# Optimization experiments

Hardware: AMD Instinct MI355X
Metric: run time of the kernel (lower is better)

The kernel has to match this reference:

```python
import jax, jax.numpy as jnp
import numpy as np

B, L, H, D = 2, 2048, 16, 64
HID = H * D
EPS = 1e-6


def setup_inputs() -> dict:
    key = jax.random.key(0)
    k1, k2, k3 = jax.random.split(key, 3)
    x = jax.random.normal(k1, (B, L, HID), dtype=jnp.float32)
    Wqkv = jax.random.normal(k2, (HID, 3 * HID), dtype=jnp.float32) * 0.02
    Wo = jax.random.normal(k3, (HID, HID), dtype=jnp.float32) * 0.02
    q_norm_w = jnp.ones((D,), dtype=jnp.float32)
    k_norm_w = jnp.ones((D,), dtype=jnp.float32)
    # real RoPE tables: (L, D/2)
    d2 = D // 2
    inv_freq = 1.0 / (10000.0 ** (np.arange(d2, dtype=np.float32) / d2))
    ang = np.arange(L, dtype=np.float32)[:, None] * inv_freq[None, :]
    cos = jnp.asarray(np.cos(ang), dtype=jnp.float32)
    sin = jnp.asarray(np.sin(ang), dtype=jnp.float32)
    return {"x": x, "Wqkv": Wqkv, "Wo": Wo, "q_norm_w": q_norm_w,
            "k_norm_w": k_norm_w, "cos": cos, "sin": sin}


def _rmsnorm(t, w, eps=EPS):
    # normalize over last (head_dim) axis
    var = jnp.mean(t * t, axis=-1, keepdims=True)
    return t * jax.lax.rsqrt(var + eps) * w


def _rope(t, cos, sin):
    # t: (B,H,L,D); cos,sin: (1,1,L,D/2)
    d2 = t.shape[-1] // 2
    t1, t2 = t[..., :d2], t[..., d2:]
    return jnp.concatenate([t1 * cos - t2 * sin, t1 * sin + t2 * cos], axis=-1)


def reference(x, Wqkv, Wo, q_norm_w, k_norm_w, cos, sin):
    Bx, Lx, _ = x.shape
    qkv = x @ Wqkv                                   # (B,L,3*HID)
    qkv = qkv.reshape(Bx, Lx, 3, H, D)
    q = jnp.transpose(qkv[:, :, 0], (0, 2, 1, 3))    # (B,H,L,D)
    k = jnp.transpose(qkv[:, :, 1], (0, 2, 1, 3))
    v = jnp.transpose(qkv[:, :, 2], (0, 2, 1, 3))
    q = _rmsnorm(q, q_norm_w)
    k = _rmsnorm(k, k_norm_w)
    c = cos[:Lx][None, None]                         # (1,1,L,D/2)
    s = sin[:Lx][None, None]
    q = _rope(q, c, s)
    k = _rope(k, c, s)
    scale = 1.0 / jnp.sqrt(jnp.float32(D))
    scores = jnp.einsum("bhqd,bhkd->bhqk", q, k) * scale
    causal = jnp.tril(jnp.ones((Lx, Lx), dtype=bool))
    scores = jnp.where(causal, scores, jnp.finfo(scores.dtype).min)
    attn = jax.nn.softmax(scores, axis=-1)
    out = jnp.einsum("bhqk,bhkd->bhqd", attn, v)     # (B,H,L,D)
    out = jnp.transpose(out, (0, 2, 1, 3)).reshape(Bx, Lx, HID)
    return out @ Wo
```

## Files before the change

### kernel.cpp

```cpp
#include <hip/hip_runtime.h>
#include <hip/hip_bf16.h>

typedef __attribute__((ext_vector_type(8))) short bh8;
typedef __attribute__((ext_vector_type(4))) float f4;

typedef unsigned short u16;
typedef unsigned int u32;

__device__ inline u16 f2b(float f) {
  __hip_bfloat16 h = __float2bfloat16(f);
  union { __hip_bfloat16 h; u16 u; } v; v.h = h; return v.u;
}
__device__ inline float b2f(u16 b) {
  union { u32 u; float f; } v; v.u = ((u32)b) << 16;
  return v.f;
}

__device__ __forceinline__ void gload16(const u16* g, u16* l) {
  __builtin_amdgcn_global_load_lds(
      (__attribute__((address_space(1))) void*)(g),
      (__attribute__((address_space(3))) void*)(l),
      16, 0, 0);
}

__global__ __launch_bounds__(256) void k_prep1(const float* __restrict__ x,
                                               const float* __restrict__ Wqkv,
                                               const float* __restrict__ Wo,
                                               u16* __restrict__ xb,
                                               u16* __restrict__ wqkvT,
                                               u16* __restrict__ woT) {
  int idx = blockIdx.x;
  if (idx < 4096) {
    int i = (idx * 256 + threadIdx.x) * 4;
    float4 v = *(const float4*)&x[i];
    ushort4 o;
    o.x = f2b(v.x); o.y = f2b(v.y); o.z = f2b(v.z); o.w = f2b(v.w);
    *(ushort4*)&xb[i] = o;
    return;
  }
  __shared__ u16 t[32][33];
  const float* W; u16* WT; int K, N, bxi, byi;
  if (idx < 7168) {
    int id2 = idx - 4096;
    W = Wqkv; WT = wqkvT; K = 1024; N = 3072;
    bxi = id2 % 96; byi = id2 / 96;
  } else {
    int id2 = idx - 7168;
    W = Wo; WT = woT; K = 1024; N = 1024;
    bxi = id2 & 31; byi = id2 >> 5;
  }
  int bx = bxi * 32, by = byi * 32;
  int xx = threadIdx.x & 31, yy = threadIdx.x >> 5;
  for (int j = 0; j < 4; ++j) {
    int r = yy + j * 8;
    t[r][xx] = f2b(W[(size_t)(by + r) * N + bx + xx]);
  }
  __syncthreads();
  for (int j = 0; j < 4; ++j) {
    int r = yy + j * 8;
    WT[(size_t)(bx + r) * K + by + xx] = t[xx][r];
  }
}

template <bool F32OUT>
__global__ __launch_bounds__(512, 2) void k_gemm256(const u16* __restrict__ A,
                                                    const u16* __restrict__ Bt,
                                                    void* __restrict__ Cout,
                                                    int M, int N, int K) {
  __shared__ u16 As[2][2][128 * 64];
  __shared__ u16 Bs[2][2][128 * 64];
  const int tid = threadIdx.x;
  const int lane = tid & 63, wid = tid >> 6;
  const int l15 = lane & 15, lg = lane >> 4;
  const int wm = wid >> 2, wn = wid & 3;

  int nwg = gridDim.x * gridDim.y;
  int bid = blockIdx.y * gridDim.x + blockIdx.x;
  int cpx = nwg >> 3;
  int swz = (bid & 7) * cpx + (bid >> 3);
  int bx = swz % gridDim.x, by = swz / gridDim.x;
  const int bm = bx * 256, bn = by * 256;

  f4 acc[8][4] = {};

  const int srow = wid * 16 + (lane >> 3);
  const int key0 = (lane >> 3) & 7;
  const int scol = ((lane & 7) ^ key0) * 8;

  const int nk = K >> 6;

#define STAGE256(T)                                                                   \
  {                                                                                   \
    int kb_ = (T) << 6; int bf_ = (T) & 1;                                            \
    _Pragma("unroll")                                                                 \
    for (int h = 0; h < 2; ++h) {                                                     \
      const u16* ga = A + (size_t)(bm + h * 128 + srow) * K + kb_ + scol;             \
      u16* la = &As[bf_][h][(wid * 16) * 64];                                         \
      gload16(ga, la);                                                                \
      gload16(ga + (size_t)8 * K, la + 8 * 64);                                       \
      const u16* gb = Bt + (size_t)(bn + h * 128 + srow) * K + kb_ + scol;            \
      u16* lb = &Bs[bf_][h][(wid * 16) * 64];                                         \
      gload16(gb, lb);                                                                \
      gload16(gb + (size_t)8 * K, lb + 8 * 64);                                       \
    }                                                                                 \
  }

#define QUAD256(T, MH, NH)                                                            \
  {                                                                                   \
    const u16* as_ = &As[(T) & 1][wm][0];                                             \
    const u16* bs_ = &Bs[(T) & 1][wn >> 1][0];                                        \
    bh8 a_[4][2], b_[2][2];                                                           \
    _Pragma("unroll")                                                                 \
    for (int i = 0; i < 4; ++i) {                                                     \
      int ar = ((MH) * 4 + i) * 16 + l15;                                             \
      _Pragma("unroll")                                                               \
      for (int kk = 0; kk < 2; ++kk)                                                  \
        a_[i][kk] = *(const bh8*)&as_[ar * 64 + (((kk * 4 + lg) ^ (ar & 7)) * 8)];    \
    }                                                                                 \
    _Pragma("unroll")                                                                 \
    for (int j = 0; j < 2; ++j) {                                                     \
      int br = (wn & 1) * 64 + ((NH) * 2 + j) * 16 + l15;                             \
      _Pragma("unroll")                                                               \
      for (int kk = 0; kk < 2; ++kk)                                                  \
        b_[j][kk] = *(const bh8*)&bs_[br * 64 + (((kk * 4 + lg) ^ (br & 7)) * 8)];    \
    }                                                                                 \
    asm volatile("s_waitcnt lgkmcnt(0)" ::: "memory");                                \
    __builtin_amdgcn_sched_barrier(0);                                                \
    __builtin_amdgcn_s_setprio(1);                                                    \
    _Pragma("unroll")                                                                 \
    for (int kk = 0; kk < 2; ++kk)                                                    \
      _Pragma("unroll")                                                               \
      for (int i = 0; i < 4; ++i)                                                     \
        _Pragma("unroll")                                                             \
        for (int j = 0; j < 2; ++j)                                                   \
          acc[(MH) * 4 + i][(NH) * 2 + j] = __builtin_amdgcn_mfma_f32_16x16x32_bf16(  \
              a_[i][kk], b_[j][kk], acc[(MH) * 4 + i][(NH) * 2 + j], 0, 0, 0);        \
    __builtin_amdgcn_s_setprio(0);                                                    \
  }

  STAGE256(0);
  __syncthreads();

  for (int t = 0; t < nk; ++t) {
    if (t + 1 < nk) STAGE256(t + 1);
    QUAD256(t, 0, 0);
    QUAD256(t, 0, 1);
    QUAD256(t, 1, 0);
    QUAD256(t, 1, 1);
    __syncthreads();
  }
#undef STAGE256
#undef QUAD256

  for (int mf = 0; mf < 8; ++mf)
    for (int nf = 0; nf < 4; ++nf)
      for (int r = 0; r < 4; ++r) {
        int row = bm + wm * 128 + mf * 16 + lg * 4 + r;
        int col = bn + wn * 64 + nf * 16 + l15;
        float v = acc[mf][nf][r];
        if constexpr (F32OUT) ((float*)Cout)[(size_t)row * N + col] = v;
        else                  ((u16*)Cout)[(size_t)row * N + col]  = f2b(v);
      }
}

template <bool F32OUT>
__global__ __launch_bounds__(256) void k_gemm(const u16* __restrict__ A,
                                              const u16* __restrict__ Bt,
                                              void* __restrict__ Cout,
                                              int M, int N, int K) {
  __shared__ u16 As[2][128 * 64];
  __shared__ u16 Bs[2][128 * 64];
  const int tid = threadIdx.x;
  const int lane = tid & 63, wid = tid >> 6;
  const int l15 = lane & 15, lg = lane >> 4;
  const int bm = blockIdx.x * 128, bn = blockIdx.y * 128;
  const int wr = (wid >> 1) * 64, wc = (wid & 1) * 64;

  f4 acc[4][4] = {};

  const int srow = wid * 32 + (lane >> 3);
  const int scol = (lane & 7) * 8;
  const u16* gA = A  + (size_t)(bm + srow) * K + scol;
  const u16* gB = Bt + (size_t)(bn + srow) * K + scol;

  const int nk = K >> 6;

  {
    const u16* ga = gA; const u16* gb = gB;
    u16* la = &As[0][(wid * 32) * 64];
    u16* lb = &Bs[0][(wid * 32) * 64];
    #pragma unroll
    for (int c = 0; c < 4; ++c) {
      gload16(ga, la);
      gload16(gb, lb);
      ga += (size_t)8 * K; gb += (size_t)8 * K;
      la += 8 * 64;        lb += 8 * 64;
    }
  }
  __syncthreads();

  for (int t = 0; t < nk; ++t) {
    if (t + 1 < nk) {
      int kb = (t + 1) << 6;
      const u16* ga = gA + kb; const u16* gb = gB + kb;
      u16* la = &As[(t + 1) & 1][(wid * 32) * 64];
      u16* lb = &Bs[(t + 1) & 1][(wid * 32) * 64];
      #pragma unroll
      for (int c = 0; c < 4; ++c) {
        gload16(ga, la);
        gload16(gb, lb);
        ga += (size_t)8 * K; gb += (size_t)8 * K;
        la += 8 * 64;        lb += 8 * 64;
      }
    }
    const u16* as = &As[t & 1][0];
    const u16* bs = &Bs[t & 1][0];
    #pragma unroll
    for (int kk = 0; kk < 2; ++kk) {
      bh8 a[4], b[4];
      #pragma unroll
      for (int m = 0; m < 4; ++m)
        a[m] = *(const bh8*)&as[(wr + m * 16 + l15) * 64 + kk * 32 + lg * 8];
      #pragma unroll
      for (int n = 0; n < 4; ++n)
        b[n] = *(const bh8*)&bs[(wc + n * 16 + l15) * 64 + kk * 32 + lg * 8];
      #pragma unroll
      for (int m = 0; m < 4; ++m)
        #pragma unroll
        for (int n = 0; n < 4; ++n)
          acc[m][n] = __builtin_amdgcn_mfma_f32_16x16x32_bf16(a[m], b[n], acc[m][n], 0, 0, 0);
    }
    __syncthreads();
  }

  for (int m = 0; m < 4; ++m)
    for (int n = 0; n < 4; ++n)
      for (int r = 0; r < 4; ++r) {
        int row = bm + wr + m * 16 + lg * 4 + r;
        int col = bn + wc + n * 16 + l15;
        float v = acc[m][n][r];
        if constexpr (F32OUT) ((float*)Cout)[(size_t)row * N + col] = v;
        else                  ((u16*)Cout)[(size_t)row * N + col]  = f2b(v);
      }
}

__global__ __launch_bounds__(256) void k_prep2(const u16* __restrict__ qkv,
                                               const float* __restrict__ qw,
                                               const float* __restrict__ kw,
                                               const float* __restrict__ cosp,
                                               const float* __restrict__ sinp,
                                               u16* __restrict__ Q,
                                               u16* __restrict__ K,
                                               u16* __restrict__ Vt) {
  const float CSC = 0.125f * 1.44269504088896f;
  int idx = blockIdx.x;
  if (idx < 2048) {
    int wid = threadIdx.x >> 6, lane = threadIdx.x & 63;
    int gw = idx * 4 + wid;
    int isK = gw & 1;
    int bl = gw >> 1;
    int l = bl & 2047, b = bl >> 11;
    int h = lane >> 2, qd = lane & 3;
    const u16* src = qkv + (size_t)bl * 3072 + isK * 1024 + h * 64 + qd * 8;
    bh8 t1 = *(const bh8*)src;
    bh8 t2 = *(const bh8*)(src + 32);
    float a1[8], a2[8];
    float ss = 0.0f;
    #pragma unroll
    for (int j = 0; j < 8; ++j) {
      a1[j] = b2f((u16)t1[j]); a2[j] = b2f((u16)t2[j]);
      ss += a1[j] * a1[j] + a2[j] * a2[j];
    }
    ss += __shfl_xor(ss, 1, 64);
    ss += __shfl_xor(ss, 2, 64);
    float rr = rsqrtf(ss * (1.0f / 64.0f) + 1e-6f);
    const float* wt = isK ? kw : qw;
    float w1[8], w2[8], cc[8], sn[8];
    *(float4*)&w1[0] = *(const float4*)&wt[qd * 8];
    *(float4*)&w1[4] = *(const float4*)&wt[qd * 8 + 4];
    *(float4*)&w2[0] = *(const float4*)&wt[32 + qd * 8];
    *(float4*)&w2[4] = *(const float4*)&wt[32 + qd * 8 + 4];
    *(float4*)&cc[0] = *(const float4*)&cosp[l * 32 + qd * 8];
    *(float4*)&cc[4] = *(const float4*)&cosp[l * 32 + qd * 8 + 4];
    *(float4*)&sn[0] = *(const float4*)&sinp[l * 32 + qd * 8];
    *(float4*)&sn[4] = *(const float4*)&sinp[l * 32 + qd * 8 + 4];
    float scl = isK ? 1.0f : CSC;
    bh8 o1, o2;
    #pragma unroll
    for (int j = 0; j < 8; ++j) {
      float x1 = a1[j] * rr * w1[j];
      float x2 = a2[j] * rr * w2[j];
      o1[j] = (short)f2b((x1 * cc[j] - x2 * sn[j]) * scl);
      o2[j] = (short)f2b((x1 * sn[j] + x2 * cc[j]) * scl);
    }
    u16* dst = (isK ? K : Q) + ((size_t)(b * 16 + h) * 2048 + l) * 64 + qd * 8;
    *(bh8*)dst = o1;
    *(bh8*)(dst + 32) = o2;
  } else {
    __shared__ u16 t[32][33];
    int v = idx - 2048;
    int bxi = v & 63, byi = (v >> 6) & 1, bh = v >> 7;
    int b = bh >> 4, h = bh & 15;
    int lb = bxi * 32, db = byi * 32;
    int xx = threadIdx.x & 31, yy = threadIdx.x >> 5;
    const u16* src = qkv + (size_t)b * 2048 * 3072 + 2048 + h * 64;
    for (int j = 0; j < 4; ++j) {
      int r = yy + j * 8;
      t[r][xx] = src[(size_t)(lb + r) * 3072 + db + xx];
    }
    __syncthreads();
    u16* dst = Vt + (size_t)bh * 64 * 2048;
    for (int j = 0; j < 4; ++j) {
      int r = yy + j * 8;
      dst[(size_t)(db + r) * 2048 + lb + xx] = t[xx][r];
    }
  }
}

__global__ __launch_bounds__(256, 3) void k_attn(const u16* __restrict__ Q,
                                                 const u16* __restrict__ K,
                                                 const u16* __restrict__ Vt,
                                                 u16* __restrict__ O,
                                                 u16* __restrict__ Opart,
                                                 float2* __restrict__ Ml) {
  __shared__ u16 Ks[2][64 * 64];
  __shared__ u16 Vs[2][64 * 64];
  __shared__ u16 Pl[4][32][64];

  const int bh = blockIdx.y;
  const int b = bh >> 4, h = bh & 15;
  const int wid = threadIdx.x >> 6, lane = threadIdx.x & 63;
  const int l15 = lane & 15, lg = lane >> 4;

  const int id = 39 - (int)blockIdx.x;
  int qt, t0, t1, slot;
  if (id < 4) { qt = id; t0 = 0; t1 = 2 * qt + 2; slot = -1; }
  else if (id < 12) {
    int p = id - 4; qt = 4 + (p >> 1); int half = p & 1;
    int nt = qt + 1; t0 = half * nt; t1 = t0 + nt;
    slot = bh * 36 + (qt - 4) * 2 + half;
  } else if (id < 24) {
    int p = id - 12; qt = 8 + p / 3; int part = p % 3;
    int T = 2 * qt + 2; t0 = part * T / 3; t1 = (part + 1) * T / 3;
    slot = bh * 36 + 8 + (qt - 8) * 3 + part;
  } else {
    int p = id - 24; qt = 12 + (p >> 2); int part = p & 3;
    int T = 2 * qt + 2; t0 = part * T / 4; t1 = (part + 1) * T / 4;
    slot = bh * 36 + 20 + (qt - 12) * 4 + part;
  }
  const int qb = qt * 128 + wid * 32;

  const u16* Qp = Q  + (size_t)bh * 2048 * 64;
  const u16* Kp = K  + (size_t)bh * 2048 * 64;
  const u16* Vp = Vt + (size_t)bh * 64 * 2048;

  const int sr0 = wid * 8 + (lane >> 3);
  const int sc  = lane & 7;

  bh8 aq[2][2];
  #pragma unroll
  for (int qi = 0; qi < 2; ++qi)
    #pragma unroll
    for (int hh = 0; hh < 2; ++hh)
      aq[qi][hh] = *(const bh8*)&Qp[(size_t)(qb + qi * 16 + l15) * 64 + hh * 32 + lg * 8];

  bh8 ones;
  #pragma unroll
  for (int j = 0; j < 8; ++j) ones[j] = (short)0x3F80;

  f4 acc[2][4] = {};
  float mrow[2] = {-1e30f, -1e30f};
  float lrow[2] = {0.0f, 0.0f};

  const int tmax = (qb + 31) >> 6;

  {
    int kb0 = t0 * 64;
    int r0 = sr0, r1 = 32 + sr0;
    gload16(Kp + (size_t)(kb0 + r0) * 64 + (size_t)((sc ^ (r0 & 7)) * 8), &Ks[t0 & 1][(wid * 8) * 64]);
    gload16(Kp + (size_t)(kb0 + r1) * 64 + (size_t)((sc ^ (r1 & 7)) * 8), &Ks[t0 & 1][(32 + wid * 8) * 64]);
    gload16(Vp + (size_t)r0 * 2048 + kb0 + (size_t)((sc ^ (r0 & 7)) * 8), &Vs[t0 & 1][(wid * 8) * 64]);
    gload16(Vp + (size_t)r1 * 2048 + kb0 + (size_t)((sc ^ (r1 & 7)) * 8), &Vs[t0 & 1][(32 + wid * 8) * 64]);
  }
  __syncthreads();

  for (int t = t0; t < t1; ++t) {
    if (t + 1 < t1) {
      int kb = (t + 1) * 64;
      int nb = (t + 1) & 1;
      int r0 = sr0, r1 = 32 + sr0;
      gload16(Kp + (size_t)(kb + r0) * 64 + (size_t)((sc ^ (r0 & 7)) * 8), &Ks[nb][(wid * 8) * 64]);
      gload16(Kp + (size_t)(kb + r1) * 64 + (size_t)((sc ^ (r1 & 7)) * 8), &Ks[nb][(32 + wid * 8) * 64]);
      gload16(Vp + (size_t)r0 * 2048 + kb + (size_t)((sc ^ (r0 & 7)) * 8), &Vs[nb][(wid * 8) * 64]);
      gload16(Vp + (size_t)r1 * 2048 + kb + (size_t)((sc ^ (r1 & 7)) * 8), &Vs[nb][(32 + wid * 8) * 64]);
    }
    if (t <= tmax) {
      const int kb = t * 64;
      const bool masked = (t == tmax);
      const u16* ks = &Ks[t & 1][0];
      const u16* vs = &Vs[t & 1][0];

      f4 sc4[4][2] = {};
      __builtin_amdgcn_s_setprio(1);
      #pragma unroll
      for (int kq = 0; kq < 4; ++kq) {
        int row = kq * 16 + l15;
        int cs = row & 7;
        bh8 ka0 = *(const bh8*)&ks[row * 64 + ((0 + lg) ^ cs) * 8];
        bh8 ka1 = *(const bh8*)&ks[row * 64 + ((4 + lg) ^ cs) * 8];
        #pragma unroll
        for (int qi = 0; qi < 2; ++qi) {
          sc4[kq][qi] = __builtin_amdgcn_mfma_f32_16x16x32_bf16(ka0, aq[qi][0], sc4[kq][qi], 0, 0, 0);
          sc4[kq][qi] = __builtin_amdgcn_mfma_f32_16x16x32_bf16(ka1, aq[qi][1], sc4[kq][qi], 0, 0, 0);
        }
      }
      __builtin_amdgcn_s_setprio(0);

      #pragma unroll
      for (int qi = 0; qi < 2; ++qi) {
        if (masked) {
          int q = qb + qi * 16 + l15;
          #pragma unroll
          for (int kq = 0; kq < 4; ++kq)
            #pragma unroll
            for (int r = 0; r < 4; ++r)
              if (kb + kq * 16 + lg * 4 + r > q) sc4[kq][qi][r] = -1e30f;
        }
        float mx = -1e30f;
        #pragma unroll
        for (int kq = 0; kq < 4; ++kq)
          #pragma unroll
          for (int r = 0; r < 4; ++r)
            mx = fmaxf(mx, sc4[kq][qi][r]);
        mx = fmaxf(mx, __shfl_xor(mx, 16, 64));
        mx = fmaxf(mx, __shfl_xor(mx, 32, 64));
        if (__any(mx > mrow[qi] + 8.0f)) {
          float mnew = fmaxf(mrow[qi], mx);
          float fac = exp2f(mrow[qi] - mnew);
          mrow[qi] = mnew;
          lrow[qi] *= fac;
          #pragma unroll
          for (int n = 0; n < 4; ++n)
            #pragma unroll
            for (int r = 0; r < 4; ++r) acc[qi][n][r] *= fac;
        }
        #pragma unroll
        for (int kq = 0; kq < 4; ++kq)
          #pragma unroll
          for (int r = 0; r < 4; ++r)
            sc4[kq][qi][r] = exp2f(sc4[kq][qi][r] - mrow[qi]);
      }

      char* plb = (char*)&Pl[wid][0][0];
      #pragma unroll
      for (int qi = 0; qi < 2; ++qi) {
        int row = qi * 16 + l15;
        #pragma unroll
        for (int kq = 0; kq < 4; ++kq) {
          ushort4 w4;
          w4.x = f2b(sc4[kq][qi][0]); w4.y = f2b(sc4[kq][qi][1]);
          w4.z = f2b(sc4[kq][qi][2]); w4.w = f2b(sc4[kq][qi][3]);
          int ch = (kq * 2 + (lg >> 1)) ^ (row & 7);
          *(ushort4*)(plb + row * 128 + ch * 16 + (lg & 1) * 8) = w4;
        }
      }
      asm volatile("s_waitcnt lgkmcnt(0)" ::: "memory");
      __builtin_amdgcn_sched_barrier(0);

      f4 sum0 = {}, sum1 = {};
      __builtin_amdgcn_s_setprio(1);
      #pragma unroll
      for (int g = 0; g < 2; ++g) {
        bh8 pb0 = *(const bh8*)(plb + l15 * 128 + (((g * 4 + lg) ^ (l15 & 7)) * 16));
        bh8 pb1 = *(const bh8*)(plb + (16 + l15) * 128 + (((g * 4 + lg) ^ (l15 & 7)) * 16));
        #pragma unroll
        for (int n = 0; n < 4; ++n) {
          int row = n * 16 + l15;
          bh8 va = *(const bh8*)&vs[row * 64 + (((g * 4 + lg) ^ (row & 7)) * 8)];
          acc[0][n] = __builtin_amdgcn_mfma_f32_16x16x32_bf16(va, pb0, acc[0][n], 0, 0, 0);
          acc[1][n] = __builtin_amdgcn_mfma_f32_16x16x32_bf16(va, pb1, acc[1][n], 0, 0, 0);
        }
        sum0 = __builtin_amdgcn_mfma_f32_16x16x32_bf16(ones, pb0, sum0, 0, 0, 0);
        sum1 = __builtin_amdgcn_mfma_f32_16x16x32_bf16(ones, pb1, sum1, 0, 0, 0);
      }
      __builtin_amdgcn_s_setprio(0);
      lrow[0] += sum0[0];
      lrow[1] += sum1[0];
    }
    __syncthreads();
  }

  if (slot < 0) {
    #pragma unroll
    for (int qi = 0; qi < 2; ++qi) {
      float inv = 1.0f / lrow[qi];
      int q = qb + qi * 16 + l15;
      #pragma unroll
      for (int n = 0; n < 4; ++n) {
        ushort4 w4;
        w4.x = f2b(acc[qi][n][0] * inv);
        w4.y = f2b(acc[qi][n][1] * inv);
        w4.z = f2b(acc[qi][n][2] * inv);
        w4.w = f2b(acc[qi][n][3] * inv);
        *(ushort4*)&O[((size_t)b * 2048 + q) * 1024 + h * 64 + n * 16 + lg * 4] = w4;
      }
    }
  } else {
    u16* op = Opart + (size_t)slot * 8192;
    #pragma unroll
    for (int qi = 0; qi < 2; ++qi) {
      int rloc = wid * 32 + qi * 16 + l15;
      #pragma unroll
      for (int n = 0; n < 4; ++n) {
        ushort4 w4;
        w4.x = f2b(acc[qi][n][0]); w4.y = f2b(acc[qi][n][1]);
        w4.z = f2b(acc[qi][n][2]); w4.w = f2b(acc[qi][n][3]);
        *(ushort4*)&op[(size_t)rloc * 64 + n * 16 + lg * 4] = w4;
      }
      if (lg == 0) Ml[slot * 128 + rloc] = make_float2(mrow[qi], lrow[qi]);
    }
  }
}

__global__ __launch_bounds__(256) void k_comb(const u16* __restrict__ Opart,
                                              const float2* __restrict__ Ml,
                                              u16* __restrict__ O) {
  int qt = 4 + (int)blockIdx.x;
  int bh = blockIdx.y;
  int b = bh >> 4, h = bh & 15;
  int ways = qt < 8 ? 2 : (qt < 12 ? 3 : 4);
  int base = bh * 36 + (qt < 8 ? (qt - 4) * 2 : qt < 12 ? 8 + (qt - 8) * 3 : 20 + (qt - 12) * 4);
  int row = threadIdx.x >> 1;
  int db  = (threadIdx.x & 1) * 32;

  float2 ml[4]; float wgt[4];
  float M = -1e30f;
  #pragma unroll
  for (int w = 0; w < 4; ++w)
    if (w < ways) { ml[w] = Ml[(base + w) * 128 + row]; M = fmaxf(M, ml[w].x); }
  float l = 0.0f;
  #pragma unroll
  for (int w = 0; w < 4; ++w)
    if (w < ways) { wgt[w] = exp2f(ml[w].x - M); l += wgt[w] * ml[w].y; }
  float inv = 1.0f / l;

  u16* dst = O + ((size_t)b * 2048 + qt * 128 + row) * 1024 + h * 64 + db;
  #pragma unroll
  for (int j = 0; j < 32; j += 8) {
    float a[8] = {};
    #pragma unroll
    for (int w = 0; w < 4; ++w)
      if (w < ways) {
        bh8 v = *(const bh8*)&Opart[(size_t)(base + w) * 8192 + (size_t)row * 64 + db + j];
        #pragma unroll
        for (int e = 0; e < 8; ++e) a[e] += wgt[w] * b2f((u16)v[e]);
      }
    bh8 o;
    #pragma unroll
    for (int e = 0; e < 8; ++e) o[e] = (short)f2b(a[e] * inv);
    *(bh8*)&dst[j] = o;
  }
}

extern "C" void kernel_launch(void* const* d_in, const int* in_sizes, int n_in,
                              void* d_out, int out_size, void* d_ws, size_t ws_size,
                              hipStream_t stream) {
  (void)in_sizes; (void)n_in; (void)out_size; (void)ws_size;
  const float* x    = (const float*)d_in[0];
  const float* Wqkv = (const float*)d_in[1];
  const float* Wo   = (const float*)d_in[2];
  const float* qw   = (const float*)d_in[3];
  const float* kw   = (const float*)d_in[4];
  const float* cosp = (const float*)d_in[5];
  const float* sinp = (const float*)d_in[6];
  float* out = (float*)d_out;

  char* ws = (char*)d_ws;
  u16* xb    = (u16*)(ws);
  u16* wqkvT = (u16*)(ws + 8388608);
  u16* woT   = (u16*)(ws + 14680064);
  u16* qkv   = (u16*)(ws + 16777216);
  u16* Qb    = (u16*)(ws + 41943040);
  u16* Kb    = (u16*)(ws + 50331648);
  u16* Vtb   = (u16*)(ws + 58720256);
  u16* AO    = (u16*)(ws + 67108864);
  u16*    Opart = (u16*)(ws + 16777216);
  float2* Mlb   = (float2*)(ws + 35651584);

  k_prep1<<<8192, 256, 0, stream>>>(x, Wqkv, Wo, xb, wqkvT, woT);
  k_gemm256<false><<<dim3(16, 12), 512, 0, stream>>>(xb, wqkvT, qkv, 4096, 3072, 1024);
  k_prep2<<<6144, 256, 0, stream>>>(qkv, qw, kw, cosp, sinp, Qb, Kb, Vtb);
  k_attn<<<dim3(40, 32), 256, 0, stream>>>(Qb, Kb, Vtb, AO, Opart, Mlb);
  k_comb<<<dim3(12, 32), 256, 0, stream>>>(Opart, Mlb, AO);
  k_gemm<true><<<dim3(32, 8), 256, 0, stream>>>(AO, woT, out, 4096, 1024, 1024);
}
```

Measured before the change: 144.1 us.

## Enlarge attention query tile to 256 rows with 8 waves, swizzle GEMM LDS

The attention kernel now uses 512-thread blocks covering 256 query rows, so each K/V tile loaded into shared memory is reused by eight waves instead of four. The split-K schedule and the combine kernel are rewritten for the coarser query tiles (18 partial slots per head, one thread per row). Separately, the output GEMM's LDS layout gets an XOR swizzle on 16-byte chunks to avoid bank conflicts on fragment reads. The trade-offs are fewer, larger attention blocks, which means lower occupancy and coarser load balancing across CUs, and more partial output per slot.

Result: slower. 161.1 us (+11.8%).

```diff
diff --git a/kernel.cpp b/kernel.cpp
--- a/kernel.cpp
+++ b/kernel.cpp
@@ -179,7 +179,7 @@
   f4 acc[4][4] = {};
 
   const int srow = wid * 32 + (lane >> 3);
-  const int scol = (lane & 7) * 8;
+  const int scol = ((lane & 7) ^ ((lane >> 3) & 7)) * 8;
   const u16* gA = A  + (size_t)(bm + srow) * K + scol;
   const u16* gB = Bt + (size_t)(bn + srow) * K + scol;
 
@@ -220,10 +220,10 @@
       bh8 a[4], b[4];
       #pragma unroll
       for (int m = 0; m < 4; ++m)
-        a[m] = *(const bh8*)&as[(wr + m * 16 + l15) * 64 + kk * 32 + lg * 8];
+        a[m] = *(const bh8*)&as[(wr + m * 16 + l15) * 64 + (((kk * 4 + lg) ^ (l15 & 7)) * 8)];
       #pragma unroll
       for (int n = 0; n < 4; ++n)
-        b[n] = *(const bh8*)&bs[(wc + n * 16 + l15) * 64 + kk * 32 + lg * 8];
+        b[n] = *(const bh8*)&bs[(wc + n * 16 + l15) * 64 + (((kk * 4 + lg) ^ (l15 & 7)) * 8)];
       #pragma unroll
       for (int m = 0; m < 4; ++m)
         #pragma unroll
@@ -317,7 +317,7 @@
   }
 }
 
-__global__ __launch_bounds__(256, 3) void k_attn(const u16* __restrict__ Q,
+__global__ __launch_bounds__(512, 2) void k_attn(const u16* __restrict__ Q,
                                                  const u16* __restrict__ K,
                                                  const u16* __restrict__ Vt,
                                                  u16* __restrict__ O,
@@ -325,37 +325,37 @@
                                                  float2* __restrict__ Ml) {
   __shared__ u16 Ks[2][64 * 64];
   __shared__ u16 Vs[2][64 * 64];
-  __shared__ u16 Pl[4][32][64];
+  __shared__ u16 Pl[8][32][64];
 
   const int bh = blockIdx.y;
   const int b = bh >> 4, h = bh & 15;
   const int wid = threadIdx.x >> 6, lane = threadIdx.x & 63;
   const int l15 = lane & 15, lg = lane >> 4;
 
-  const int id = 39 - (int)blockIdx.x;
+  const int id = 19 - (int)blockIdx.x;
   int qt, t0, t1, slot;
-  if (id < 4) { qt = id; t0 = 0; t1 = 2 * qt + 2; slot = -1; }
-  else if (id < 12) {
-    int p = id - 4; qt = 4 + (p >> 1); int half = p & 1;
-    int nt = qt + 1; t0 = half * nt; t1 = t0 + nt;
-    slot = bh * 36 + (qt - 4) * 2 + half;
-  } else if (id < 24) {
-    int p = id - 12; qt = 8 + p / 3; int part = p % 3;
-    int T = 2 * qt + 2; t0 = part * T / 3; t1 = (part + 1) * T / 3;
-    slot = bh * 36 + 8 + (qt - 8) * 3 + part;
+  if (id < 2) { qt = id; t0 = 0; t1 = 4 * qt + 4; slot = -1; }
+  else if (id < 6) {
+    int p = id - 2; qt = 2 + (p >> 1); int part = p & 1;
+    int T = 4 * qt + 4; t0 = part * T / 2; t1 = (part + 1) * T / 2;
+    slot = bh * 18 + (qt - 2) * 2 + part;
+  } else if (id < 12) {
+    int p = id - 6; qt = 4 + p / 3; int part = p % 3;
+    int T = 4 * qt + 4; t0 = part * T / 3; t1 = (part + 1) * T / 3;
+    slot = bh * 18 + 4 + (qt - 4) * 3 + part;
   } else {
-    int p = id - 24; qt = 12 + (p >> 2); int part = p & 3;
-    int T = 2 * qt + 2; t0 = part * T / 4; t1 = (part + 1) * T / 4;
-    slot = bh * 36 + 20 + (qt - 12) * 4 + part;
-  }
-  const int qb = qt * 128 + wid * 32;
+    int p = id - 12; qt = 6 + (p >> 2); int part = p & 3;
+    int T = 4 * qt + 4; t0 = part * T / 4; t1 = (part + 1) * T / 4;
+    slot = bh * 18 + 10 + (qt - 6) * 4 + part;
+  }
+  const int qb = qt * 256 + wid * 32;
 
   const u16* Qp = Q  + (size_t)bh * 2048 * 64;
   const u16* Kp = K  + (size_t)bh * 2048 * 64;
   const u16* Vp = Vt + (size_t)bh * 64 * 2048;
 
-  const int sr0 = wid * 8 + (lane >> 3);
-  const int sc  = lane & 7;
+  const int sr = wid * 8 + (lane >> 3);
+  const int sc = lane & 7;
 
   bh8 aq[2][2];
   #pragma unroll
@@ -376,11 +376,8 @@
 
   {
     int kb0 = t0 * 64;
-    int r0 = sr0, r1 = 32 + sr0;
-    gload16(Kp + (size_t)(kb0 + r0) * 64 + (size_t)((sc ^ (r0 & 7)) * 8), &Ks[t0 & 1][(wid * 8) * 64]);
-    gload16(Kp + (size_t)(kb0 + r1) * 64 + (size_t)((sc ^ (r1 & 7)) * 8), &Ks[t0 & 1][(32 + wid * 8) * 64]);
-    gload16(Vp + (size_t)r0 * 2048 + kb0 + (size_t)((sc ^ (r0 & 7)) * 8), &Vs[t0 & 1][(wid * 8) * 64]);
-    gload16(Vp + (size_t)r1 * 2048 + kb0 + (size_t)((sc ^ (r1 & 7)) * 8), &Vs[t0 & 1][(32 + wid * 8) * 64]);
+    gload16(Kp + (size_t)(kb0 + sr) * 64 + (size_t)((sc ^ (sr & 7)) * 8), &Ks[t0 & 1][(wid * 8) * 64]);
+    gload16(Vp + (size_t)sr * 2048 + kb0 + (size_t)((sc ^ (sr & 7)) * 8), &Vs[t0 & 1][(wid * 8) * 64]);
   }
   __syncthreads();
 
@@ -388,11 +385,8 @@
     if (t + 1 < t1) {
       int kb = (t + 1) * 64;
       int nb = (t + 1) & 1;
-      int r0 = sr0, r1 = 32 + sr0;
-      gload16(Kp + (size_t)(kb + r0) * 64 + (size_t)((sc ^ (r0 & 7)) * 8), &Ks[nb][(wid * 8) * 64]);
-      gload16(Kp + (size_t)(kb + r1) * 64 + (size_t)((sc ^ (r1 & 7)) * 8), &Ks[nb][(32 + wid * 8) * 64]);
-      gload16(Vp + (size_t)r0 * 2048 + kb + (size_t)((sc ^ (r0 & 7)) * 8), &Vs[nb][(wid * 8) * 64]);
-      gload16(Vp + (size_t)r1 * 2048 + kb + (size_t)((sc ^ (r1 & 7)) * 8), &Vs[nb][(32 + wid * 8) * 64]);
+      gload16(Kp + (size_t)(kb + sr) * 64 + (size_t)((sc ^ (sr & 7)) * 8), &Ks[nb][(wid * 8) * 64]);
+      gload16(Vp + (size_t)sr * 2048 + kb + (size_t)((sc ^ (sr & 7)) * 8), &Vs[nb][(wid * 8) * 64]);
     }
     if (t <= tmax) {
       const int kb = t * 64;
@@ -506,7 +500,7 @@
       }
     }
   } else {
-    u16* op = Opart + (size_t)slot * 8192;
+    u16* op = Opart + (size_t)slot * 16384;
     #pragma unroll
     for (int qi = 0; qi < 2; ++qi) {
       int rloc = wid * 32 + qi * 16 + l15;
@@ -517,7 +511,7 @@
         w4.z = f2b(acc[qi][n][2]); w4.w = f2b(acc[qi][n][3]);
         *(ushort4*)&op[(size_t)rloc * 64 + n * 16 + lg * 4] = w4;
       }
-      if (lg == 0) Ml[slot * 128 + rloc] = make_float2(mrow[qi], lrow[qi]);
+      if (lg == 0) Ml[slot * 256 + rloc] = make_float2(mrow[qi], lrow[qi]);
     }
   }
 }
@@ -525,33 +519,32 @@
 __global__ __launch_bounds__(256) void k_comb(const u16* __restrict__ Opart,
                                               const float2* __restrict__ Ml,
                                               u16* __restrict__ O) {
-  int qt = 4 + (int)blockIdx.x;
+  int qt = 2 + (int)blockIdx.x;
   int bh = blockIdx.y;
   int b = bh >> 4, h = bh & 15;
-  int ways = qt < 8 ? 2 : (qt < 12 ? 3 : 4);
-  int base = bh * 36 + (qt < 8 ? (qt - 4) * 2 : qt < 12 ? 8 + (qt - 8) * 3 : 20 + (qt - 12) * 4);
-  int row = threadIdx.x >> 1;
-  int db  = (threadIdx.x & 1) * 32;
+  int ways = qt < 4 ? 2 : (qt < 6 ? 3 : 4);
+  int base = bh * 18 + (qt < 4 ? (qt - 2) * 2 : qt < 6 ? 4 + (qt - 4) * 3 : 10 + (qt - 6) * 4);
+  int row = threadIdx.x;
 
   float2 ml[4]; float wgt[4];
   float M = -1e30f;
   #pragma unroll
   for (int w = 0; w < 4; ++w)
-    if (w < ways) { ml[w] = Ml[(base + w) * 128 + row]; M = fmaxf(M, ml[w].x); }
+    if (w < ways) { ml[w] = Ml[(base + w) * 256 + row]; M = fmaxf(M, ml[w].x); }
   float l = 0.0f;
   #pragma unroll
   for (int w = 0; w < 4; ++w)
     if (w < ways) { wgt[w] = exp2f(ml[w].x - M); l += wgt[w] * ml[w].y; }
   float inv = 1.0f / l;
 
-  u16* dst = O + ((size_t)b * 2048 + qt * 128 + row) * 1024 + h * 64 + db;
+  u16* dst = O + ((size_t)b * 2048 + qt * 256 + row) * 1024 + h * 64;
   #pragma unroll
-  for (int j = 0; j < 32; j += 8) {
+  for (int j = 0; j < 64; j += 8) {
     float a[8] = {};
     #pragma unroll
     for (int w = 0; w < 4; ++w)
       if (w < ways) {
-        bh8 v = *(const bh8*)&Opart[(size_t)(base + w) * 8192 + (size_t)row * 64 + db + j];
+        bh8 v = *(const bh8*)&Opart[(size_t)(base + w) * 16384 + (size_t)row * 64 + j];
         #pragma unroll
         for (int e = 0; e < 8; ++e) a[e] += wgt[w] * b2f((u16)v[e]);
       }
@@ -590,7 +583,7 @@
   k_prep1<<<8192, 256, 0, stream>>>(x, Wqkv, Wo, xb, wqkvT, woT);
   k_gemm256<false><<<dim3(16, 12), 512, 0, stream>>>(xb, wqkvT, qkv, 4096, 3072, 1024);
   k_prep2<<<6144, 256, 0, stream>>>(qkv, qw, kw, cosp, sinp, Qb, Kb, Vtb);
-  k_attn<<<dim3(40, 32), 256, 0, stream>>>(Qb, Kb, Vtb, AO, Opart, Mlb);
-  k_comb<<<dim3(12, 32), 256, 0, stream>>>(Opart, Mlb, AO);
+  k_attn<<<dim3(20, 32), 512, 0, stream>>>(Qb, Kb, Vtb, AO, Opart, Mlb);
+  k_comb<<<dim3(6, 32), 256, 0, stream>>>(Opart, Mlb, AO);
   k_gemm<true><<<dim3(32, 8), 256, 0, stream>>>(AO, woT, out, 4096, 1024, 1024);
 }
```

## Swizzle output GEMM LDS layout and rebalance attention split-K partitioning

Applied to the files above, without the earlier changes.

The output-projection GEMM now XOR-swizzles the 16-byte chunk column when loading tiles into LDS and when reading MFMA fragments, to cut LDS bank conflicts. The attention kernel swaps its hard-coded 1/2/3/4-way split of causal query tiles for a table-driven partition with up to 5 ways, giving 46 blocks per head instead of 40 for finer load balance. The combine kernel and the workspace offsets are updated to match the new slot count. The change adds more partial outputs to merge and a small table lookup per block.

New measurement: 142.6 us. No clear change (-1.0%).

```diff
diff --git a/kernel.cpp b/kernel.cpp
--- a/kernel.cpp
+++ b/kernel.cpp
@@ -179,7 +179,7 @@
   f4 acc[4][4] = {};
 
   const int srow = wid * 32 + (lane >> 3);
-  const int scol = (lane & 7) * 8;
+  const int scol = ((lane & 7) ^ ((lane >> 3) & 7)) * 8;
   const u16* gA = A  + (size_t)(bm + srow) * K + scol;
   const u16* gB = Bt + (size_t)(bn + srow) * K + scol;
 
@@ -220,10 +220,10 @@
       bh8 a[4], b[4];
       #pragma unroll
       for (int m = 0; m < 4; ++m)
-        a[m] = *(const bh8*)&as[(wr + m * 16 + l15) * 64 + kk * 32 + lg * 8];
+        a[m] = *(const bh8*)&as[(wr + m * 16 + l15) * 64 + (((kk * 4 + lg) ^ (l15 & 7)) * 8)];
       #pragma unroll
       for (int n = 0; n < 4; ++n)
-        b[n] = *(const bh8*)&bs[(wc + n * 16 + l15) * 64 + kk * 32 + lg * 8];
+        b[n] = *(const bh8*)&bs[(wc + n * 16 + l15) * 64 + (((kk * 4 + lg) ^ (l15 & 7)) * 8)];
       #pragma unroll
       for (int m = 0; m < 4; ++m)
         #pragma unroll
@@ -332,22 +332,19 @@
   const int wid = threadIdx.x >> 6, lane = threadIdx.x & 63;
   const int l15 = lane & 15, lg = lane >> 4;
 
-  const int id = 39 - (int)blockIdx.x;
-  int qt, t0, t1, slot;
-  if (id < 4) { qt = id; t0 = 0; t1 = 2 * qt + 2; slot = -1; }
-  else if (id < 12) {
-    int p = id - 4; qt = 4 + (p >> 1); int half = p & 1;
-    int nt = qt + 1; t0 = half * nt; t1 = t0 + nt;
-    slot = bh * 36 + (qt - 4) * 2 + half;
-  } else if (id < 24) {
-    int p = id - 12; qt = 8 + p / 3; int part = p % 3;
-    int T = 2 * qt + 2; t0 = part * T / 3; t1 = (part + 1) * T / 3;
-    slot = bh * 36 + 8 + (qt - 8) * 3 + part;
-  } else {
-    int p = id - 24; qt = 12 + (p >> 2); int part = p & 3;
-    int T = 2 * qt + 2; t0 = part * T / 4; t1 = (part + 1) * T / 4;
-    slot = bh * 36 + 20 + (qt - 12) * 4 + part;
-  }
+  const int ctab[17] = {0,1,2,3,5,7,9,11,14,17,20,24,28,32,36,41,46};
+  const int id = 45 - (int)blockIdx.x;
+  int qt = 0;
+  #pragma unroll
+  for (int qq = 0; qq < 16; ++qq)
+    if (id >= ctab[qq + 1]) qt = qq + 1;
+  const int part = id - ctab[qt];
+  const int ways = ctab[qt + 1] - ctab[qt];
+  const int T = 2 * qt + 2;
+  const int t0 = part * T / ways;
+  const int t1 = (part + 1) * T / ways;
+  const int slot = (ways == 1) ? -1 : bh * 43 + (id - 3);
+
   const int qb = qt * 128 + wid * 32;
 
   const u16* Qp = Q  + (size_t)bh * 2048 * 64;
@@ -525,22 +522,23 @@
 __global__ __launch_bounds__(256) void k_comb(const u16* __restrict__ Opart,
                                               const float2* __restrict__ Ml,
                                               u16* __restrict__ O) {
-  int qt = 4 + (int)blockIdx.x;
+  const int ctab[17] = {0,1,2,3,5,7,9,11,14,17,20,24,28,32,36,41,46};
+  int qt = 3 + (int)blockIdx.x;
   int bh = blockIdx.y;
   int b = bh >> 4, h = bh & 15;
-  int ways = qt < 8 ? 2 : (qt < 12 ? 3 : 4);
-  int base = bh * 36 + (qt < 8 ? (qt - 4) * 2 : qt < 12 ? 8 + (qt - 8) * 3 : 20 + (qt - 12) * 4);
+  int ways = ctab[qt + 1] - ctab[qt];
+  int base = bh * 43 + ctab[qt] - 3;
   int row = threadIdx.x >> 1;
   int db  = (threadIdx.x & 1) * 32;
 
-  float2 ml[4]; float wgt[4];
+  float2 ml[5]; float wgt[5];
   float M = -1e30f;
   #pragma unroll
-  for (int w = 0; w < 4; ++w)
+  for (int w = 0; w < 5; ++w)
     if (w < ways) { ml[w] = Ml[(base + w) * 128 + row]; M = fmaxf(M, ml[w].x); }
   float l = 0.0f;
   #pragma unroll
-  for (int w = 0; w < 4; ++w)
+  for (int w = 0; w < 5; ++w)
     if (w < ways) { wgt[w] = exp2f(ml[w].x - M); l += wgt[w] * ml[w].y; }
   float inv = 1.0f / l;
 
@@ -549,7 +547,7 @@
   for (int j = 0; j < 32; j += 8) {
     float a[8] = {};
     #pragma unroll
-    for (int w = 0; w < 4; ++w)
+    for (int w = 0; w < 5; ++w)
       if (w < ways) {
         bh8 v = *(const bh8*)&Opart[(size_t)(base + w) * 8192 + (size_t)row * 64 + db + j];
         #pragma unroll
@@ -585,12 +583,12 @@
   u16* Vtb   = (u16*)(ws + 58720256);
   u16* AO    = (u16*)(ws + 67108864);
   u16*    Opart = (u16*)(ws + 16777216);
-  float2* Mlb   = (float2*)(ws + 35651584);
+  float2* Mlb   = (float2*)(ws + 16777216 + 22544384);
 
   k_prep1<<<8192, 256, 0, stream>>>(x, Wqkv, Wo, xb, wqkvT, woT);
   k_gemm256<false><<<dim3(16, 12), 512, 0, stream>>>(xb, wqkvT, qkv, 4096, 3072, 1024);
   k_prep2<<<6144, 256, 0, stream>>>(qkv, qw, kw, cosp, sinp, Qb, Kb, Vtb);
-  k_attn<<<dim3(40, 32), 256, 0, stream>>>(Qb, Kb, Vtb, AO, Opart, Mlb);
-  k_comb<<<dim3(12, 32), 256, 0, stream>>>(Opart, Mlb, AO);
+  k_attn<<<dim3(46, 32), 256, 0, stream>>>(Qb, Kb, Vtb, AO, Opart, Mlb);
+  k_comb<<<dim3(13, 32), 256, 0, stream>>>(Opart, Mlb, AO);
   k_gemm<true><<<dim3(32, 8), 256, 0, stream>>>(AO, woT, out, 4096, 1024, 1024);
 }
```
